# Kernel optimization log

Measured on AMD Instinct MI355X. Metric: run time of the kernel, lower is better.

The kernel has to match this reference:

```python
import jax, jax.numpy as jnp
import numpy as np

N = 100000
E = 1_600_000
DIN = 24
DH = 64
DOUT = 12
NEG_SLOPE = 0.01  # torch F.leaky_relu default


def setup_inputs() -> dict:
    key = jax.random.key(0)
    ks = jax.random.split(key, 18)
    inp = {}
    inp["feats"] = jax.random.normal(ks[0], (N, DIN), dtype=jnp.float32)
    inp["e_w"] = jax.random.uniform(ks[1], (E, 1), dtype=jnp.float32)
    inp["snorm_n"] = jnp.ones((N, 1), dtype=jnp.float32)
    inp["snorm_e"] = jnp.ones((E, 1), dtype=jnp.float32)
    inp["src"] = jax.random.randint(ks[2], (E,), 0, N, dtype=jnp.int32)
    inp["dst"] = jax.random.randint(ks[3], (E,), 0, N, dtype=jnp.int32)
    s = 0.05
    inp["emb_h_W"] = jax.random.normal(ks[4], (DH, DIN), dtype=jnp.float32) * s
    inp["emb_h_b"] = jnp.zeros((DH,), dtype=jnp.float32)
    inp["emb_e_W"] = jax.random.normal(ks[5], (DH, 1), dtype=jnp.float32) * s
    inp["emb_e_b"] = jnp.zeros((DH,), dtype=jnp.float32)
    inp["W_self1"] = jax.random.normal(ks[6], (DH, DH), dtype=jnp.float32) * s
    inp["W_func1"] = jax.random.normal(ks[7], (DH, DH), dtype=jnp.float32) * s
    inp["attn1"] = jax.random.normal(ks[8], (3 * DH,), dtype=jnp.float32) * s
    inp["W_self2"] = jax.random.normal(ks[9], (DH, DH), dtype=jnp.float32) * s
    inp["W_func2"] = jax.random.normal(ks[10], (DH, DH), dtype=jnp.float32) * s
    inp["attn2"] = jax.random.normal(ks[11], (3 * DH,), dtype=jnp.float32) * s
    inp["lin1_W"] = jax.random.normal(ks[12], (DOUT, DH), dtype=jnp.float32) * s
    inp["lin1_b"] = jnp.zeros((DOUT,), dtype=jnp.float32)
    return inp


def _gat_layer(h, w_edge, src, dst, W_self, W_func, attn):
    # h: [N, d], w_edge: [E, d] edge embedding, attn: [3d]
    h_s = h @ W_self.T                       # linear_self(h)
    z = h @ W_func.T                         # linear_func(h)
    d = z.shape[-1]
    a_src, a_dst, a_w = attn[:d], attn[d:2 * d], attn[2 * d:]
    # attention score: W_a . [z_src, z_dst, w]  (decomposed to avoid [E,3d] concat)
    s_node_src = z @ a_src                   # [N]
    s_node_dst = z @ a_dst                   # [N]
    e = s_node_src[src] + s_node_dst[dst] + w_edge @ a_w  # [E]
    e = jax.nn.leaky_relu(e, NEG_SLOPE)
    # segment softmax over incoming edges per destination node
    m = jax.ops.segment_max(e, dst, num_segments=h.shape[0])
    ex = jnp.exp(e - m[dst])
    denom = jax.ops.segment_sum(ex, dst, num_segments=h.shape[0])
    alpha = ex / denom[dst]                  # [E]
    msg = alpha[:, None] * z[src]            # [E, d]
    agg = jax.ops.segment_sum(msg, dst, num_segments=h.shape[0])  # [N, d]
    # DGL: nodes with no incoming edges keep their old 'h' (not h_s + agg)
    in_deg = jax.ops.segment_sum(jnp.ones_like(e), dst, num_segments=h.shape[0])
    h_mid = jnp.where((in_deg > 0)[:, None], h_s + agg, h)
    return h + jax.nn.relu(h_mid)            # relu then residual


def reference(feats, e_w, snorm_n, snorm_e, src, dst,
              emb_h_W, emb_h_b, emb_e_W, emb_e_b,
              W_self1, W_func1, attn1, W_self2, W_func2, attn2,
              lin1_W, lin1_b):
    feats = feats.reshape(feats.shape[0], -1)
    h = feats @ emb_h_W.T + emb_h_b          # [N, DH]
    e = e_w @ emb_e_W.T + emb_e_b            # [E, DH]
    h = _gat_layer(h, e, src, dst, W_self1, W_func1, attn1)
    h = _gat_layer(h, e, src, dst, W_self2, W_func2, attn2)
    y = h @ lin1_W.T + lin1_b                # [N, DOUT]
    return y
```

## Files before the change

### kernel.cpp

```cpp
#include <hip/hip_runtime.h>
#include <hip/hip_fp16.h>

#define N_NODES 100000
#define N_EDGES 1600000
#define DIN 24
#define DH 64
#define DOUT 12
#define NEG_SLOPE 0.01f
#define NG 32
#define EPG (N_EDGES / NG)
#define NS 7
#define SLICE_N 16384
#define NTOT (NG * N_NODES)
#define SCAN_BLK 4096
#define LDSW 72

#define NB_HIST (NS * NG)
#define NB_EMBED ((N_NODES * DH) / 1024)
#define NB_SCAN1G ((NTOT + SCAN_BLK - 1) / SCAN_BLK)
#define NB_SUMDEG ((N_NODES + 255) / 256)
#define NB_SCAN1N ((N_NODES + SCAN_BLK - 1) / SCAN_BLK)
#define NB_SCAN3G ((NTOT + 255) / 256)
#define NB_SCATTER (NG * 32)
#define BPE ((EPG + 31) / 32)
#define NB_NODE ((N_NODES + 63) / 64)
#define NB_SCAN3N ((N_NODES + 255) / 256)
#define NB_COMPACT ((N_NODES + 7) / 8)
#define NB_AGG ((N_NODES + 7) / 8)

typedef _Float16 half8_t __attribute__((ext_vector_type(8)));
typedef float floatx4 __attribute__((ext_vector_type(4)));

__device__ __forceinline__ void dev_consts(const float* emb_e_W, const float* emb_e_b,
                                           const float* attn1, const float* attn2,
                                           float* consts) {
    int lane = threadIdx.x;
    if (lane >= 64) return;
    float w = emb_e_W[lane], b = emb_e_b[lane];
    float a1 = attn1[2 * DH + lane], a2 = attn2[2 * DH + lane];
    float c11 = w * a1, c01 = b * a1, c12 = w * a2, c02 = b * a2;
    for (int off = 32; off; off >>= 1) {
        c11 += __shfl_down(c11, off);
        c01 += __shfl_down(c01, off);
        c12 += __shfl_down(c12, off);
        c02 += __shfl_down(c02, off);
    }
    if (lane == 0) {
        consts[0] = c11; consts[1] = c01; consts[2] = c12; consts[3] = c02;
    }
}

__device__ __forceinline__ void dev_hist(int bid, const int* dst,
                                         unsigned char* deg, unsigned char* rank) {
    __shared__ unsigned cnt[SLICE_N / 4];
    int s = bid % NS, c = bid / NS;
    for (int i = threadIdx.x; i < SLICE_N / 4; i += 1024) cnt[i] = 0;
    __syncthreads();
    int nbase = s * SLICE_N;
    int start = c * EPG, end = start + EPG;
    for (int i = start + threadIdx.x; i < end; i += 1024) {
        int local = dst[i] - nbase;
        if ((unsigned)local < SLICE_N) {
            unsigned sh = (unsigned)(local & 3) * 8u;
            unsigned old = atomicAdd(&cnt[local >> 2], 1u << sh);
            rank[i] = (unsigned char)((old >> sh) & 255u);
        }
    }
    __syncthreads();
    int nmax = N_NODES - nbase;
    if (nmax > SLICE_N) nmax = SLICE_N;
    unsigned* dw = (unsigned*)(deg + (size_t)c * N_NODES + nbase);
    for (int l = threadIdx.x; l < (nmax >> 2); l += 1024) dw[l] = cnt[l];
}

__device__ __forceinline__ void dev_embed(int bid, const float* feats, const float* W,
                                          const float* b, float* h) {
    int idx = bid * 1024 + threadIdx.x;
    if (idx >= N_NODES * DH) return;
    int n = idx >> 6, o = idx & 63;
    const float* f = feats + n * DIN;
    const float* w = W + o * DIN;
    float acc = b[o];
#pragma unroll
    for (int k = 0; k < DIN; ++k) acc += f[k] * w[k];
    h[idx] = acc;
}

__device__ __forceinline__ void dev_scan1B(int bid, const unsigned* inW,
                                           unsigned short* out, int* part, int n) {
    __shared__ int lds[256];
    int t = threadIdx.x;
    int base = bid * SCAN_BLK + t * 16;
    unsigned wv[4];
#pragma unroll
    for (int i = 0; i < 4; ++i) wv[i] = inW[(base >> 2) + i];
    int v[16];
    int s = 0;
#pragma unroll
    for (int i = 0; i < 16; ++i) {
        int idx = base + i;
        int c = (int)((wv[i >> 2] >> ((i & 3) * 8)) & 255u);
        v[i] = (idx < n) ? c : 0;
        s += v[i];
    }
    lds[t] = s;
    __syncthreads();
    for (int off = 1; off < 256; off <<= 1) {
        int y = (t >= off) ? lds[t - off] : 0;
        __syncthreads();
        lds[t] += y;
        __syncthreads();
    }
    int run = lds[t] - s;
#pragma unroll
    for (int i = 0; i < 16; ++i) {
        int idx = base + i;
        if (idx < n) out[idx] = (unsigned short)run;
        run += v[i];
    }
    if (t == 255) part[bid] = lds[255];
}

__device__ __forceinline__ void dev_scan1(int bid, const int* in, int* out,
                                          int* part, int n) {
    __shared__ int lds[256];
    int t = threadIdx.x;
    int base = bid * SCAN_BLK + t * 16;
    int v[16];
    int s = 0;
#pragma unroll
    for (int i = 0; i < 16; ++i) {
        int idx = base + i;
        v[i] = (idx < n) ? in[idx] : 0;
        s += v[i];
    }
    lds[t] = s;
    __syncthreads();
    for (int off = 1; off < 256; off <<= 1) {
        int y = (t >= off) ? lds[t - off] : 0;
        __syncthreads();
        lds[t] += y;
        __syncthreads();
    }
    int run = lds[t] - s;
#pragma unroll
    for (int i = 0; i < 16; ++i) {
        int idx = base + i;
        if (idx < n) out[idx] = run;
        run += v[i];
    }
    if (t == 255) part[bid] = lds[255];
}

__device__ __forceinline__ void dev_scan2(int* part, int nblk) {
    __shared__ int lds2[256];
    int t = threadIdx.x;
    int v[4];
    int s = 0;
#pragma unroll
    for (int i = 0; i < 4; ++i) {
        int idx = t * 4 + i;
        v[i] = (idx < nblk) ? part[idx] : 0;
        s += v[i];
    }
    lds2[t] = s;
    __syncthreads();
    for (int off = 1; off < 256; off <<= 1) {
        int y = (t >= off) ? lds2[t - off] : 0;
        __syncthreads();
        lds2[t] += y;
        __syncthreads();
    }
    int run = lds2[t] - s;
#pragma unroll
    for (int i = 0; i < 4; ++i) {
        int idx = t * 4 + i;
        if (idx < nblk) part[idx] = run;
        run += v[i];
    }
}

__device__ __forceinline__ void dev_sumdeg(int bid, const unsigned char* degB, int* degN) {
    int n = bid * 256 + threadIdx.x;
    if (n >= N_NODES) return;
    int s = 0;
#pragma unroll
    for (int g = 0; g < NG; ++g) s += (int)degB[(size_t)g * N_NODES + n];
    degN[n] = s;
}

__device__ __forceinline__ void dev_scatter(int bid, const int* src, const int* dst,
                                            const float* e_w, const unsigned char* rank,
                                            const unsigned short* row_offG, unsigned* csr) {
    int g = bid & 31, q = bid >> 5;
    int start = g * EPG + q * BPE;
    int end = start + BPE;
    int gend = (g + 1) * EPG;
    if (end > gend) end = gend;
    const unsigned short* ro = row_offG + (size_t)g * N_NODES;
    int cbase = g * EPG;
    for (int i = start + threadIdx.x; i < end; i += 256) {
        int d = dst[i];
        unsigned qv = (unsigned)(e_w[i] * 32768.f);
        if (qv > 32767u) qv = 32767u;
        unsigned w = (unsigned)src[i] | (qv << 17);
        int pos = cbase + (int)ro[d] + (int)rank[i];
        csr[pos] = w;
    }
}

__device__ __forceinline__ void dev_node(int bid, const float* h,
                                         const float* Wself, const float* Wfunc,
                                         const float* attn,
                                         __half* zh, float* hs,
                                         float* s_src, float* s_dst) {
    __shared__ _Float16 lds[2 * 64 * LDSW];
    int tid = threadIdx.x;
    for (int idx = tid; idx < 2 * 64 * 64; idx += 256) {
        int mat = idx >> 12, rem = idx & 4095;
        int o = rem >> 6, k = rem & 63;
        float v = mat ? Wfunc[rem] : Wself[rem];
        lds[(mat * 64 + o) * LDSW + k] = (_Float16)v;
    }
    __syncthreads();

    int wave = tid >> 6, lane = tid & 63;
    int n0 = (bid * 4 + wave) * 16;
    if (n0 >= N_NODES) return;
    int quad = lane >> 4, lm = lane & 15;

    half8_t afrag[2];
    {
        const float4* hrow = (const float4*)(h + (size_t)(n0 + lm) * DH);
#pragma unroll
        for (int ks = 0; ks < 2; ++ks) {
            float4 p0 = hrow[ks * 8 + quad * 2];
            float4 p1 = hrow[ks * 8 + quad * 2 + 1];
            half8_t a;
            a[0] = (_Float16)p0.x; a[1] = (_Float16)p0.y;
            a[2] = (_Float16)p0.z; a[3] = (_Float16)p0.w;
            a[4] = (_Float16)p1.x; a[5] = (_Float16)p1.y;
            a[6] = (_Float16)p1.z; a[7] = (_Float16)p1.w;
            afrag[ks] = a;
        }
    }

    floatx4 accS[4], accF[4];
#pragma unroll
    for (int t = 0; t < 4; ++t) { accS[t] = (floatx4)0.f; accF[t] = (floatx4)0.f; }

    const _Float16* bS = lds;
    const _Float16* bF = lds + 64 * LDSW;
#pragma unroll
    for (int t = 0; t < 4; ++t) {
        int o = t * 16 + lm;
#pragma unroll
        for (int ks = 0; ks < 2; ++ks) {
            int hoff = o * LDSW + ks * 32 + quad * 8;
            half8_t b1 = *(const half8_t*)(bS + hoff);
            half8_t b2 = *(const half8_t*)(bF + hoff);
            accS[t] = __builtin_amdgcn_mfma_f32_16x16x32_f16(afrag[ks], b1, accS[t], 0, 0, 0);
            accF[t] = __builtin_amdgcn_mfma_f32_16x16x32_f16(afrag[ks], b2, accF[t], 0, 0, 0);
        }
    }

    float asv[4], adv[4];
#pragma unroll
    for (int t = 0; t < 4; ++t) {
        asv[t] = attn[t * 16 + lm];
        adv[t] = attn[DH + t * 16 + lm];
    }
    float ps[4] = {0.f, 0.f, 0.f, 0.f}, pd[4] = {0.f, 0.f, 0.f, 0.f};
#pragma unroll
    for (int t = 0; t < 4; ++t) {
#pragma unroll
        for (int r = 0; r < 4; ++r) {
            int node = n0 + quad * 4 + r;
            float zv = accF[t][r];
            zh[(size_t)node * DH + t * 16 + lm] = __float2half(zv);
            hs[(size_t)node * DH + t * 16 + lm] = accS[t][r];
            ps[r] += zv * asv[t];
            pd[r] += zv * adv[t];
        }
    }
#pragma unroll
    for (int r = 0; r < 4; ++r) {
        float p1 = ps[r], p2 = pd[r];
        for (int off = 8; off; off >>= 1) {
            p1 += __shfl_xor(p1, off);
            p2 += __shfl_xor(p2, off);
        }
        if (lm == 0) {
            s_src[n0 + quad * 4 + r] = p1;
            s_dst[n0 + quad * 4 + r] = p2;
        }
    }
}

__global__ void __launch_bounds__(1024, 2)
k_fuse1(const float* __restrict__ feats, const float* __restrict__ emb_h_W,
        const float* __restrict__ emb_h_b, float* __restrict__ h,
        const int* __restrict__ dst, unsigned char* __restrict__ deg,
        unsigned char* __restrict__ rank,
        const float* __restrict__ emb_e_W, const float* __restrict__ emb_e_b,
        const float* __restrict__ attn1, const float* __restrict__ attn2,
        float* __restrict__ consts) {
    int bid = blockIdx.x;
    if (bid == 0) { dev_consts(emb_e_W, emb_e_b, attn1, attn2, consts); return; }
    bid -= 1;
    if (bid < NB_HIST) { dev_hist(bid, dst, deg, rank); return; }
    dev_embed(bid - NB_HIST, feats, emb_h_W, emb_h_b, h);
}

__global__ void k_fuse2(const unsigned* __restrict__ degW, unsigned short* __restrict__ row_offG,
                        int* __restrict__ partG, int* __restrict__ degN) {
    int bid = blockIdx.x;
    if (bid < NB_SCAN1G) { dev_scan1B(bid, degW, row_offG, partG, NTOT); return; }
    dev_sumdeg(bid - NB_SCAN1G, (const unsigned char*)degW, degN);
}

__global__ void k_fuse3(int* __restrict__ partG, const int* __restrict__ degN,
                        int* __restrict__ row_offN, int* __restrict__ partN) {
    int bid = blockIdx.x;
    if (bid == 0) { dev_scan2(partG, NB_SCAN1G); return; }
    dev_scan1(bid - 1, degN, row_offN, partN, N_NODES);
}

__global__ void k_fuse4(unsigned short* __restrict__ row_offG, const int* __restrict__ partG,
                        int* __restrict__ partN) {
    int bid = blockIdx.x;
    if (bid == 0) { dev_scan2(partN, NB_SCAN1N); return; }
    int i = (bid - 1) * 256 + threadIdx.x;
    if (i >= NTOT) return;
    int c = i / N_NODES;
    int v = (int)row_offG[i] + partG[i >> 12] - c * EPG;
    row_offG[i] = (unsigned short)v;
}

__global__ void __launch_bounds__(256, 4)
k_fuse5(const int* __restrict__ src, const int* __restrict__ dst,
        const float* __restrict__ e_w, const unsigned char* __restrict__ rank,
        const unsigned short* __restrict__ row_offG, unsigned* __restrict__ csr,
        int* __restrict__ row_offN, const int* __restrict__ partN,
        const float* __restrict__ h, const float* __restrict__ Wself1,
        const float* __restrict__ Wfunc1, const float* __restrict__ attn1,
        __half* __restrict__ zh, float* __restrict__ hs,
        float* __restrict__ s_src, float* __restrict__ s_dst) {
    int bid = blockIdx.x;
    if (bid < NB_SCATTER) { dev_scatter(bid, src, dst, e_w, rank, row_offG, csr); return; }
    bid -= NB_SCATTER;
    if (bid < NB_NODE) { dev_node(bid, h, Wself1, Wfunc1, attn1, zh, hs, s_src, s_dst); return; }
    int i = (bid - NB_NODE) * 256 + threadIdx.x;
    if (i >= N_NODES) return;
    row_offN[i] += partN[i / SCAN_BLK];
    if (i == 0) row_offN[N_NODES] = N_EDGES;
}

__global__ void k_compact(const unsigned short* __restrict__ row_offG,
                          const unsigned char* __restrict__ degB,
                          const int* __restrict__ row_offN,
                          const unsigned* __restrict__ csr, unsigned* __restrict__ csr2) {
    int wave = threadIdx.x >> 6, lane = threadIdx.x & 63;
    int n0 = (blockIdx.x * 4 + wave) * 2;
    if (n0 >= N_NODES) return;
    int g = lane & 31, nl = lane >> 5;
    int n = n0 + nl;
    int offG = 0, dg = 0;
    if (n < N_NODES) {
        size_t idx = (size_t)g * N_NODES + n;
        offG = g * EPG + (int)row_offG[idx];
        dg = (int)degB[idx];
    }
    int x = dg;
#pragma unroll
    for (int s = 1; s < 32; s <<= 1) {
        int y = __shfl_up(x, s);
        if ((lane & 31) >= s) x += y;
    }
    if (n < N_NODES) {
        int base = row_offN[n] + (x - dg);
        for (int j = 0; j < dg; ++j) csr2[base + j] = csr[offG + j];
    }
}

__global__ void __launch_bounds__(256, 4)
k_nodeL(const float* __restrict__ h, const float* __restrict__ Wself,
        const float* __restrict__ Wfunc, const float* __restrict__ attn,
        __half* __restrict__ zh, float* __restrict__ hs,
        float* __restrict__ s_src, float* __restrict__ s_dst) {
    dev_node(blockIdx.x, h, Wself, Wfunc, attn, zh, hs, s_src, s_dst);
}

__global__ void k_agg(const int* __restrict__ row_off, const unsigned* __restrict__ csr,
                      const float* __restrict__ s_src, const float* __restrict__ s_dstA,
                      const float* __restrict__ consts, int layer,
                      const __half* __restrict__ zh, const float* __restrict__ hsb,
                      float* __restrict__ h,
                      const float* __restrict__ lin_W, const float* __restrict__ lin_b,
                      float* __restrict__ y, int final_layer) {
    int wave = threadIdx.x >> 6, lane = threadIdx.x & 63;
    int half = lane >> 5, hl = lane & 31;
    int eg = (lane >> 3) & 3, c8 = lane & 7;
    int n = blockIdx.x * 8 + wave * 2 + half;
    if (n >= N_NODES) return;
    int rs = row_off[n], deg = row_off[n + 1] - rs;
    int degO = __shfl_xor(deg, 32);
    int degmax = deg > degO ? deg : degO;

    float c1 = consts[layer * 2 + 0];
    float c0 = consts[layer * 2 + 1];
    float sd = s_dstA[n];

    float acc[8];
#pragma unroll
    for (int k = 0; k < 8; ++k) acc[k] = 0.f;
    float ssl = 0.f;
    int lbase = lane & 32;

    for (int base = 0; base < degmax; base += 32) {
        float ex = 0.f;
        int s0 = 0;
        int idx = base + hl;
        if (idx < deg) {
            unsigned w = csr[rs + idx];
            s0 = (int)(w & 0x1FFFFu);
            float ew = (float)(w >> 17) * (1.f / 32768.f);
            float e = s_src[s0] + sd + ew * c1 + c0;
            e = (e > 0.f) ? e : NEG_SLOPE * e;
            ex = __expf(e);
        }
        ssl += ex;
        int cnt = degmax - base;
        if (cnt > 32) cnt = 32;
#pragma unroll 4
        for (int jb = 0; jb < cnt; jb += 4) {
            int srcl = lbase + jb + eg;
            int sj = __shfl(s0, srcl);
            float exj = __shfl(ex, srcl);
            half8_t zv = *(const half8_t*)(zh + ((size_t)sj << 6) + (c8 << 3));
#pragma unroll
            for (int k = 0; k < 8; ++k) acc[k] += exj * (float)zv[k];
        }
    }
#pragma unroll
    for (int k = 0; k < 8; ++k) {
        acc[k] += __shfl_xor(acc[k], 8);
        acc[k] += __shfl_xor(acc[k], 16);
    }
    ssl += __shfl_xor(ssl, 16); ssl += __shfl_xor(ssl, 8);
    ssl += __shfl_xor(ssl, 4);  ssl += __shfl_xor(ssl, 2);
    ssl += __shfl_xor(ssl, 1);

    const float4* hp = (const float4*)(h + (size_t)n * DH);
    float4 ho0 = hp[c8 * 2], ho1 = hp[c8 * 2 + 1];
    float hold[8] = {ho0.x, ho0.y, ho0.z, ho0.w, ho1.x, ho1.y, ho1.z, ho1.w};
    float hnew[8];
    if (deg == 0) {
#pragma unroll
        for (int k = 0; k < 8; ++k) hnew[k] = hold[k] + fmaxf(hold[k], 0.f);
    } else {
        float rinv = 1.f / ssl;
        const float4* sp = (const float4*)(hsb + (size_t)n * DH);
        float4 hs0 = sp[c8 * 2], hs1 = sp[c8 * 2 + 1];
        float hsv[8] = {hs0.x, hs0.y, hs0.z, hs0.w, hs1.x, hs1.y, hs1.z, hs1.w};
#pragma unroll
        for (int k = 0; k < 8; ++k)
            hnew[k] = hold[k] + fmaxf(hsv[k] + acc[k] * rinv, 0.f);
    }

    if (!final_layer) {
        if (eg == 0) {
            float4* op = (float4*)(h + (size_t)n * DH);
            op[c8 * 2]     = make_float4(hnew[0], hnew[1], hnew[2], hnew[3]);
            op[c8 * 2 + 1] = make_float4(hnew[4], hnew[5], hnew[6], hnew[7]);
        }
    } else {
#pragma unroll
        for (int t = 0; t < 3; ++t) {
            int o = eg * 3 + t;
            const float* wr = lin_W + o * DH + c8 * 8;
            float p = 0.f;
#pragma unroll
            for (int k = 0; k < 8; ++k) p += hnew[k] * wr[k];
            p += __shfl_xor(p, 1); p += __shfl_xor(p, 2); p += __shfl_xor(p, 4);
            if (c8 == 0) y[n * DOUT + o] = p + lin_b[o];
        }
    }
}

extern "C" void kernel_launch(void* const* d_in, const int* in_sizes, int n_in,
                              void* d_out, int out_size, void* d_ws, size_t ws_size,
                              hipStream_t stream) {
    const float* feats   = (const float*)d_in[0];
    const float* e_w     = (const float*)d_in[1];
    const int*   src     = (const int*)d_in[4];
    const int*   dst     = (const int*)d_in[5];
    const float* emb_h_W = (const float*)d_in[6];
    const float* emb_h_b = (const float*)d_in[7];
    const float* emb_e_W = (const float*)d_in[8];
    const float* emb_e_b = (const float*)d_in[9];
    const float* Wself[2] = {(const float*)d_in[10], (const float*)d_in[13]};
    const float* Wfunc[2] = {(const float*)d_in[11], (const float*)d_in[14]};
    const float* attn[2]  = {(const float*)d_in[12], (const float*)d_in[15]};
    const float* lin1_W  = (const float*)d_in[16];
    const float* lin1_b  = (const float*)d_in[17];
    float* y = (float*)d_out;

    char* ws = (char*)d_ws;
    size_t off = 0;
    auto alloc = [&](size_t bytes) {
        void* p = ws + off;
        off += (bytes + 255) & ~(size_t)255;
        return p;
    };
    float*          h        = (float*)alloc((size_t)N_NODES * DH * 4);
    __half*         zh       = (__half*)alloc((size_t)N_NODES * DH * 2);
    float*          hs       = (float*)alloc((size_t)N_NODES * DH * 4);
    unsigned*       csr      = (unsigned*)alloc((size_t)N_EDGES * 4);
    unsigned*       csr2     = (unsigned*)alloc((size_t)N_EDGES * 4);
    float*          s_src    = (float*)alloc((size_t)N_NODES * 4);
    float*          s_dst    = (float*)alloc((size_t)N_NODES * 4);
    unsigned short* row_offG = (unsigned short*)alloc((size_t)(NTOT + 128) * 2);
    int*            row_offN = (int*)alloc((size_t)(N_NODES + 1) * 4);
    unsigned char*  deg      = (unsigned char*)alloc((size_t)NTOT + 8192);
    unsigned char*  rank     = (unsigned char*)alloc((size_t)N_EDGES);
    int*            degN     = (int*)alloc((size_t)N_NODES * 4);
    int*            partG    = (int*)alloc(1024 * 4);
    int*            partN    = (int*)alloc(1024 * 4);
    float*          consts   = (float*)alloc(4 * 4);

    k_fuse1<<<1 + NB_HIST + NB_EMBED, 1024, 0, stream>>>(feats, emb_h_W, emb_h_b, h,
                                                         dst, deg, rank, emb_e_W, emb_e_b,
                                                         attn[0], attn[1], consts);
    k_fuse2<<<NB_SCAN1G + NB_SUMDEG, 256, 0, stream>>>((const unsigned*)deg, row_offG,
                                                       partG, degN);
    k_fuse3<<<1 + NB_SCAN1N, 256, 0, stream>>>(partG, degN, row_offN, partN);
    k_fuse4<<<1 + NB_SCAN3G, 256, 0, stream>>>(row_offG, partG, partN);
    k_fuse5<<<NB_SCATTER + NB_NODE + NB_SCAN3N, 256, 0, stream>>>(
        src, dst, e_w, rank, row_offG, csr, row_offN, partN,
        h, Wself[0], Wfunc[0], attn[0], zh, hs, s_src, s_dst);
    k_compact<<<NB_COMPACT, 256, 0, stream>>>(row_offG, deg, row_offN, csr, csr2);
    k_agg<<<NB_AGG, 256, 0, stream>>>(row_offN, csr2, s_src, s_dst, consts, 0,
                                      zh, hs, h, lin1_W, lin1_b, y, 0);
    k_nodeL<<<NB_NODE, 256, 0, stream>>>(h, Wself[1], Wfunc[1], attn[1],
                                         zh, hs, s_src, s_dst);
    k_agg<<<NB_AGG, 256, 0, stream>>>(row_offN, csr2, s_src, s_dst, consts, 1,
                                      zh, hs, h, lin1_W, lin1_b, y, 1);
}
```

Baseline: 345.4 us.

## Scatter edges directly into final CSR via per-chunk node offsets, drop compaction pass

```diff
diff --git a/kernel.cpp b/kernel.cpp
--- a/kernel.cpp
+++ b/kernel.cpp
@@ -16,16 +16,12 @@
 #define LDSW 72
 
 #define NB_HIST (NS * NG)
-#define NB_EMBED ((N_NODES * DH) / 1024)
-#define NB_SCAN1G ((NTOT + SCAN_BLK - 1) / SCAN_BLK)
+#define NB_EMBED (((N_NODES * DH) + 8191) / 8192)
 #define NB_SUMDEG ((N_NODES + 255) / 256)
 #define NB_SCAN1N ((N_NODES + SCAN_BLK - 1) / SCAN_BLK)
-#define NB_SCAN3G ((NTOT + 255) / 256)
 #define NB_SCATTER (NG * 32)
 #define BPE ((EPG + 31) / 32)
 #define NB_NODE ((N_NODES + 63) / 64)
-#define NB_SCAN3N ((N_NODES + 255) / 256)
-#define NB_COMPACT ((N_NODES + 7) / 8)
 #define NB_AGG ((N_NODES + 7) / 8)
 
 typedef _Float16 half8_t __attribute__((ext_vector_type(8)));
@@ -75,32 +71,30 @@
 
 __device__ __forceinline__ void dev_embed(int bid, const float* feats, const float* W,
                                           const float* b, float* h) {
-    int idx = bid * 1024 + threadIdx.x;
-    if (idx >= N_NODES * DH) return;
-    int n = idx >> 6, o = idx & 63;
-    const float* f = feats + n * DIN;
-    const float* w = W + o * DIN;
-    float acc = b[o];
-#pragma unroll
-    for (int k = 0; k < DIN; ++k) acc += f[k] * w[k];
-    h[idx] = acc;
-}
-
-__device__ __forceinline__ void dev_scan1B(int bid, const unsigned* inW,
-                                           unsigned short* out, int* part, int n) {
+    for (int r = 0; r < 8; ++r) {
+        int idx = bid * 8192 + r * 1024 + threadIdx.x;
+        if (idx >= N_NODES * DH) return;
+        int n = idx >> 6, o = idx & 63;
+        const float* f = feats + n * DIN;
+        const float* w = W + o * DIN;
+        float acc = b[o];
+#pragma unroll
+        for (int k = 0; k < DIN; ++k) acc += f[k] * w[k];
+        h[idx] = acc;
+    }
+}
+
+__device__ __forceinline__ void dev_scan1(int bid, const int* in, int* out,
+                                          int* part, int n) {
     __shared__ int lds[256];
     int t = threadIdx.x;
     int base = bid * SCAN_BLK + t * 16;
-    unsigned wv[4];
-#pragma unroll
-    for (int i = 0; i < 4; ++i) wv[i] = inW[(base >> 2) + i];
     int v[16];
     int s = 0;
 #pragma unroll
     for (int i = 0; i < 16; ++i) {
         int idx = base + i;
-        int c = (int)((wv[i >> 2] >> ((i & 3) * 8)) & 255u);
-        v[i] = (idx < n) ? c : 0;
+        v[i] = (idx < n) ? in[idx] : 0;
         s += v[i];
     }
     lds[t] = s;
@@ -115,44 +109,13 @@
 #pragma unroll
     for (int i = 0; i < 16; ++i) {
         int idx = base + i;
-        if (idx < n) out[idx] = (unsigned short)run;
-        run += v[i];
-    }
-    if (t == 255) part[bid] = lds[255];
-}
-
-__device__ __forceinline__ void dev_scan1(int bid, const int* in, int* out,
-                                          int* part, int n) {
-    __shared__ int lds[256];
-    int t = threadIdx.x;
-    int base = bid * SCAN_BLK + t * 16;
-    int v[16];
-    int s = 0;
-#pragma unroll
-    for (int i = 0; i < 16; ++i) {
-        int idx = base + i;
-        v[i] = (idx < n) ? in[idx] : 0;
-        s += v[i];
-    }
-    lds[t] = s;
-    __syncthreads();
-    for (int off = 1; off < 256; off <<= 1) {
-        int y = (t >= off) ? lds[t - off] : 0;
-        __syncthreads();
-        lds[t] += y;
-        __syncthreads();
-    }
-    int run = lds[t] - s;
-#pragma unroll
-    for (int i = 0; i < 16; ++i) {
-        int idx = base + i;
         if (idx < n) out[idx] = run;
         run += v[i];
     }
     if (t == 255) part[bid] = lds[255];
 }
 
-__device__ __forceinline__ void dev_scan2(int* part, int nblk) {
+__device__ __forceinline__ void dev_scan2(int* part, int nblk, int* row_offN) {
     __shared__ int lds2[256];
     int t = threadIdx.x;
     int v[4];
@@ -178,34 +141,45 @@
         if (idx < nblk) part[idx] = run;
         run += v[i];
     }
-}
-
-__device__ __forceinline__ void dev_sumdeg(int bid, const unsigned char* degB, int* degN) {
+    if (row_offN) {
+        __syncthreads();
+        if (t == 0) row_offN[N_NODES] = N_EDGES - part[N_NODES >> 12];
+    }
+}
+
+__device__ __forceinline__ void dev_sumdeg(int bid, const unsigned char* degB,
+                                           int* degN, unsigned char* chunkOff) {
     int n = bid * 256 + threadIdx.x;
     if (n >= N_NODES) return;
-    int s = 0;
-#pragma unroll
-    for (int g = 0; g < NG; ++g) s += (int)degB[(size_t)g * N_NODES + n];
-    degN[n] = s;
+    int run = 0;
+#pragma unroll
+    for (int g = 0; g < NG; ++g) {
+        size_t idx = (size_t)g * N_NODES + n;
+        int v = (int)degB[idx];
+        chunkOff[idx] = (unsigned char)run;
+        run += v;
+    }
+    degN[n] = run;
 }
 
 __device__ __forceinline__ void dev_scatter(int bid, const int* src, const int* dst,
                                             const float* e_w, const unsigned char* rank,
-                                            const unsigned short* row_offG, unsigned* csr) {
+                                            const int* row_offN, const int* partN,
+                                            const unsigned char* chunkOff,
+                                            unsigned* csr2) {
     int g = bid & 31, q = bid >> 5;
     int start = g * EPG + q * BPE;
     int end = start + BPE;
     int gend = (g + 1) * EPG;
     if (end > gend) end = gend;
-    const unsigned short* ro = row_offG + (size_t)g * N_NODES;
-    int cbase = g * EPG;
+    const unsigned char* co = chunkOff + (size_t)g * N_NODES;
     for (int i = start + threadIdx.x; i < end; i += 256) {
         int d = dst[i];
         unsigned qv = (unsigned)(e_w[i] * 32768.f);
         if (qv > 32767u) qv = 32767u;
         unsigned w = (unsigned)src[i] | (qv << 17);
-        int pos = cbase + (int)ro[d] + (int)rank[i];
-        csr[pos] = w;
+        int pos = row_offN[d] + partN[d >> 12] + (int)co[d] + (int)rank[i];
+        csr2[pos] = w;
     }
 }
 
@@ -312,75 +286,35 @@
     dev_embed(bid - NB_HIST, feats, emb_h_W, emb_h_b, h);
 }
 
-__global__ void k_fuse2(const unsigned* __restrict__ degW, unsigned short* __restrict__ row_offG,
-                        int* __restrict__ partG, int* __restrict__ degN) {
-    int bid = blockIdx.x;
-    if (bid < NB_SCAN1G) { dev_scan1B(bid, degW, row_offG, partG, NTOT); return; }
-    dev_sumdeg(bid - NB_SCAN1G, (const unsigned char*)degW, degN);
-}
-
-__global__ void k_fuse3(int* __restrict__ partG, const int* __restrict__ degN,
-                        int* __restrict__ row_offN, int* __restrict__ partN) {
-    int bid = blockIdx.x;
-    if (bid == 0) { dev_scan2(partG, NB_SCAN1G); return; }
-    dev_scan1(bid - 1, degN, row_offN, partN, N_NODES);
-}
-
-__global__ void k_fuse4(unsigned short* __restrict__ row_offG, const int* __restrict__ partG,
+__global__ void k_prep2(const unsigned char* __restrict__ degB, int* __restrict__ degN,
+                        unsigned char* __restrict__ chunkOff) {
+    dev_sumdeg(blockIdx.x, degB, degN, chunkOff);
+}
+
+__global__ void k_prep3(const int* __restrict__ degN, int* __restrict__ row_offN,
                         int* __restrict__ partN) {
-    int bid = blockIdx.x;
-    if (bid == 0) { dev_scan2(partN, NB_SCAN1N); return; }
-    int i = (bid - 1) * 256 + threadIdx.x;
-    if (i >= NTOT) return;
-    int c = i / N_NODES;
-    int v = (int)row_offG[i] + partG[i >> 12] - c * EPG;
-    row_offG[i] = (unsigned short)v;
+    dev_scan1(blockIdx.x, degN, row_offN, partN, N_NODES);
+}
+
+__global__ void k_prep4(int* __restrict__ partN, int* __restrict__ row_offN) {
+    dev_scan2(partN, NB_SCAN1N, row_offN);
 }
 
 __global__ void __launch_bounds__(256, 4)
 k_fuse5(const int* __restrict__ src, const int* __restrict__ dst,
         const float* __restrict__ e_w, const unsigned char* __restrict__ rank,
-        const unsigned short* __restrict__ row_offG, unsigned* __restrict__ csr,
-        int* __restrict__ row_offN, const int* __restrict__ partN,
+        const int* __restrict__ row_offN, const int* __restrict__ partN,
+        const unsigned char* __restrict__ chunkOff, unsigned* __restrict__ csr2,
         const float* __restrict__ h, const float* __restrict__ Wself1,
         const float* __restrict__ Wfunc1, const float* __restrict__ attn1,
         __half* __restrict__ zh, float* __restrict__ hs,
         float* __restrict__ s_src, float* __restrict__ s_dst) {
     int bid = blockIdx.x;
-    if (bid < NB_SCATTER) { dev_scatter(bid, src, dst, e_w, rank, row_offG, csr); return; }
-    bid -= NB_SCATTER;
-    if (bid < NB_NODE) { dev_node(bid, h, Wself1, Wfunc1, attn1, zh, hs, s_src, s_dst); return; }
-    int i = (bid - NB_NODE) * 256 + threadIdx.x;
-    if (i >= N_NODES) return;
-    row_offN[i] += partN[i / SCAN_BLK];
-    if (i == 0) row_offN[N_NODES] = N_EDGES;
-}
-
-__global__ void k_compact(const unsigned short* __restrict__ row_offG,
-                          const unsigned char* __restrict__ degB,
-                          const int* __restrict__ row_offN,
-                          const unsigned* __restrict__ csr, unsigned* __restrict__ csr2) {
-    int wave = threadIdx.x >> 6, lane = threadIdx.x & 63;
-    int n0 = (blockIdx.x * 4 + wave) * 2;
-    if (n0 >= N_NODES) return;
-    int g = lane & 31, nl = lane >> 5;
-    int n = n0 + nl;
-    int offG = 0, dg = 0;
-    if (n < N_NODES) {
-        size_t idx = (size_t)g * N_NODES + n;
-        offG = g * EPG + (int)row_offG[idx];
-        dg = (int)degB[idx];
-    }
-    int x = dg;
-#pragma unroll
-    for (int s = 1; s < 32; s <<= 1) {
-        int y = __shfl_up(x, s);
-        if ((lane & 31) >= s) x += y;
-    }
-    if (n < N_NODES) {
-        int base = row_offN[n] + (x - dg);
-        for (int j = 0; j < dg; ++j) csr2[base + j] = csr[offG + j];
-    }
+    if (bid < NB_SCATTER) {
+        dev_scatter(bid, src, dst, e_w, rank, row_offN, partN, chunkOff, csr2);
+        return;
+    }
+    dev_node(bid - NB_SCATTER, h, Wself1, Wfunc1, attn1, zh, hs, s_src, s_dst);
 }
 
 __global__ void __launch_bounds__(256, 4)
@@ -391,7 +325,8 @@
     dev_node(blockIdx.x, h, Wself, Wfunc, attn, zh, hs, s_src, s_dst);
 }
 
-__global__ void k_agg(const int* __restrict__ row_off, const unsigned* __restrict__ csr,
+__global__ void k_agg(const int* __restrict__ row_off, const int* __restrict__ partN,
+                      const unsigned* __restrict__ csr,
                       const float* __restrict__ s_src, const float* __restrict__ s_dstA,
                       const float* __restrict__ consts, int layer,
                       const __half* __restrict__ zh, const float* __restrict__ hsb,
@@ -403,7 +338,9 @@
     int eg = (lane >> 3) & 3, c8 = lane & 7;
     int n = blockIdx.x * 8 + wave * 2 + half;
     if (n >= N_NODES) return;
-    int rs = row_off[n], deg = row_off[n + 1] - rs;
+    int rs = row_off[n] + partN[n >> 12];
+    int re = row_off[n + 1] + partN[(n + 1) >> 12];
+    int deg = re - rs;
     int degO = __shfl_xor(deg, 32);
     int degmax = deg > degO ? deg : degO;
 
@@ -516,34 +453,30 @@
     float*          h        = (float*)alloc((size_t)N_NODES * DH * 4);
     __half*         zh       = (__half*)alloc((size_t)N_NODES * DH * 2);
     float*          hs       = (float*)alloc((size_t)N_NODES * DH * 4);
-    unsigned*       csr      = (unsigned*)alloc((size_t)N_EDGES * 4);
     unsigned*       csr2     = (unsigned*)alloc((size_t)N_EDGES * 4);
     float*          s_src    = (float*)alloc((size_t)N_NODES * 4);
     float*          s_dst    = (float*)alloc((size_t)N_NODES * 4);
-    unsigned short* row_offG = (unsigned short*)alloc((size_t)(NTOT + 128) * 2);
     int*            row_offN = (int*)alloc((size_t)(N_NODES + 1) * 4);
-    unsigned char*  deg      = (unsigned char*)alloc((size_t)NTOT + 8192);
+    unsigned char*  deg      = (unsigned char*)alloc((size_t)NTOT + 256);
+    unsigned char*  chunkOff = (unsigned char*)alloc((size_t)NTOT + 256);
     unsigned char*  rank     = (unsigned char*)alloc((size_t)N_EDGES);
     int*            degN     = (int*)alloc((size_t)N_NODES * 4);
-    int*            partG    = (int*)alloc(1024 * 4);
     int*            partN    = (int*)alloc(1024 * 4);
     float*          consts   = (float*)alloc(4 * 4);
 
     k_fuse1<<<1 + NB_HIST + NB_EMBED, 1024, 0, stream>>>(feats, emb_h_W, emb_h_b, h,
                                                          dst, deg, rank, emb_e_W, emb_e_b,
                                                          attn[0], attn[1], consts);
-    k_fuse2<<<NB_SCAN1G + NB_SUMDEG, 256, 0, stream>>>((const unsigned*)deg, row_offG,
-                                                       partG, degN);
-    k_fuse3<<<1 + NB_SCAN1N, 256, 0, stream>>>(partG, degN, row_offN, partN);
-    k_fuse4<<<1 + NB_SCAN3G, 256, 0, stream>>>(row_offG, partG, partN);
-    k_fuse5<<<NB_SCATTER + NB_NODE + NB_SCAN3N, 256, 0, stream>>>(
-        src, dst, e_w, rank, row_offG, csr, row_offN, partN,
+    k_prep2<<<NB_SUMDEG, 256, 0, stream>>>(deg, degN, chunkOff);
+    k_prep3<<<NB_SCAN1N, 256, 0, stream>>>(degN, row_offN, partN);
+    k_prep4<<<1, 256, 0, stream>>>(partN, row_offN);
+    k_fuse5<<<NB_SCATTER + NB_NODE, 256, 0, stream>>>(
+        src, dst, e_w, rank, row_offN, partN, chunkOff, csr2,
         h, Wself[0], Wfunc[0], attn[0], zh, hs, s_src, s_dst);
-    k_compact<<<NB_COMPACT, 256, 0, stream>>>(row_offG, deg, row_offN, csr, csr2);
-    k_agg<<<NB_AGG, 256, 0, stream>>>(row_offN, csr2, s_src, s_dst, consts, 0,
+    k_agg<<<NB_AGG, 256, 0, stream>>>(row_offN, partN, csr2, s_src, s_dst, consts, 0,
                                       zh, hs, h, lin1_W, lin1_b, y, 0);
     k_nodeL<<<NB_NODE, 256, 0, stream>>>(h, Wself[1], Wfunc[1], attn[1],
                                          zh, hs, s_src, s_dst);
-    k_agg<<<NB_AGG, 256, 0, stream>>>(row_offN, csr2, s_src, s_dst, consts, 1,
+    k_agg<<<NB_AGG, 256, 0, stream>>>(row_offN, partN, csr2, s_src, s_dst, consts, 1,
                                       zh, hs, h, lin1_W, lin1_b, y, 1);
 }
```

New measurement: 314.2 us. 1.1x faster.
